# Optimization experiments

Hardware: AMD Instinct MI355X
Metric: run time of the kernel (lower is better)

The kernel has to match this reference:

```python
import jax, jax.numpy as jnp
import numpy as np

B, C, H, W = 16, 512, 64, 64   # C == e_dim
N_E = 256                       # codebook size
BETA = 0.25


def setup_inputs() -> dict:
    key = jax.random.key(0)
    k1, k2, k3 = jax.random.split(key, 3)
    z = jax.random.normal(k1, (B, C, H, W), dtype=jnp.float32)
    # nn.Embedding init: uniform(-1/n_e, 1/n_e)
    emb_weight = jax.random.uniform(k2, (N_E, C), dtype=jnp.float32,
                                    minval=-1.0 / N_E, maxval=1.0 / N_E)
    std_param = jnp.array(1.0, dtype=jnp.float32)
    means = jnp.zeros((3,), dtype=jnp.float32)
    conv_w = jax.random.normal(k3, (C, C), dtype=jnp.float32) * 0.02  # 1x1 conv kernel [out,in]
    conv_b = jnp.zeros((C,), dtype=jnp.float32)
    return {"z": z, "emb_weight": emb_weight, "std_param": std_param,
            "means": means, "conv_w": conv_w, "conv_b": conv_b}


def reference(z, emb_weight, std_param, means, conv_w, conv_b):
    # torch uses .item() on std/mean -> detached scalars
    std = jax.lax.stop_gradient(jnp.abs(std_param))
    mean = jax.lax.stop_gradient(jnp.mean(means))
    w = emb_weight * std + mean                      # [n_e, C] scaled codebook

    zf = z.transpose(0, 2, 3, 1).reshape(-1, C)       # [N, C], N = B*H*W
    # pairwise squared L2: ||z||^2 + ||w||^2 - 2 z.w
    d = (jnp.sum(zf * zf, axis=1, keepdims=True)
         + jnp.sum(w * w, axis=1)
         - 2.0 * zf @ w.T)                            # [N, n_e]
    idx = jnp.argmin(d, axis=1)                       # [N]
    one_hot = jax.nn.one_hot(idx, N_E, dtype=z.dtype) # [N, n_e]

    z_q = (one_hot @ w).reshape(B, H, W, C).transpose(0, 3, 1, 2)  # [B,C,H,W]

    sg = jax.lax.stop_gradient
    loss = jnp.mean((sg(z_q) - z) ** 2) + BETA * jnp.mean((z_q - sg(z)) ** 2)

    z_q = z + sg(z_q - z)                             # straight-through

    e_mean = jnp.mean(one_hot, axis=0)                # [n_e]
    perplexity = jnp.exp(-jnp.sum(e_mean * jnp.log(e_mean + 1e-10)))

    # 1x1 conv == channel matmul
    out = jnp.einsum('bchw,oc->bohw', z_q, conv_w) + conv_b[None, :, None, None]
    return out, loss, perplexity
```

## Files before the change

kernel.cpp:

```cpp
#include <hip/hip_runtime.h>


#define C_DIM 512
#define N_E   256
#define HW    4096
#define SAr   72

typedef unsigned short u16;
typedef u16   u16x4 __attribute__((ext_vector_type(4)));
typedef u16   u16x8 __attribute__((ext_vector_type(8)));
typedef short s16x8 __attribute__((ext_vector_type(8)));
typedef float f32x4 __attribute__((ext_vector_type(4)));

__device__ __forceinline__ u16 f2bf(float f) {
    unsigned u = __float_as_uint(f);
    return (u16)((u + 0x7FFFu + ((u >> 16) & 1u)) >> 16);
}

__global__ __launch_bounds__(256)
void prep(const float* __restrict__ emb, const float* __restrict__ stdp,
          const float* __restrict__ means, const float* __restrict__ convw,
          const float* __restrict__ convb,
          u16* __restrict__ wfrag, float* __restrict__ wnorm,
          float* __restrict__ M2T, float* __restrict__ accum,
          unsigned int* __restrict__ hist) {
    int t = threadIdx.x;
    float stdv  = fabsf(stdp[0]);
    float meanv = (means[0] + means[1] + means[2]) * (1.0f / 3.0f);

    if (blockIdx.x < 256) {
        int c = blockIdx.x;
        if (c == 0) {
            hist[t] = 0u;
            if (t < 2) accum[t] = 0.f;
        }
        float ss = 0.f;
        for (int k = t; k < C_DIM; k += 256) {
            float w = emb[c * C_DIM + k] * stdv + meanv;
            ss += w * w;
            int ntg  = c >> 4;
            int lane = (c & 15) | (((k >> 3) & 3) << 4);
            int ksg  = k >> 5;
            int j    = k & 7;
            wfrag[((ntg * 16 + ksg) * 64 + lane) * 8 + j] = f2bf(w);
        }
        #pragma unroll
        for (int m = 1; m < 64; m <<= 1) ss += __shfl_xor(ss, m, 64);
        __shared__ float red[4];
        if ((t & 63) == 0) red[t >> 6] = ss;
        __syncthreads();
        if (t == 0) wnorm[c] = red[0] + red[1] + red[2] + red[3];
    } else {
        __shared__ float cw[4][C_DIM];
        int o0 = (blockIdx.x - 256) * 4;
        for (int i = t; i < 4 * C_DIM; i += 256)
            cw[i >> 9][i & 511] = convw[(o0 + (i >> 9)) * C_DIM + (i & 511)];
        __syncthreads();
        float a0 = 0.f, a1 = 0.f, a2 = 0.f, a3 = 0.f;
        const float* er = emb + t * C_DIM;
        #pragma unroll 4
        for (int k = 0; k < C_DIM; k += 4) {
            f32x4 ev = *(const f32x4*)(er + k);
            #pragma unroll
            for (int jj = 0; jj < 4; ++jj) {
                float w = ev[jj] * stdv + meanv;
                a0 += cw[0][k + jj] * w;
                a1 += cw[1][k + jj] * w;
                a2 += cw[2][k + jj] * w;
                a3 += cw[3][k + jj] * w;
            }
        }
        M2T[(o0 + 0) * N_E + t] = a0 + convb[o0 + 0];
        M2T[(o0 + 1) * N_E + t] = a1 + convb[o0 + 1];
        M2T[(o0 + 2) * N_E + t] = a2 + convb[o0 + 2];
        M2T[(o0 + 3) * N_E + t] = a3 + convb[o0 + 3];
    }
}

__global__ __launch_bounds__(256, 4)
void argmin_out(const float* __restrict__ z, const u16* __restrict__ wfrag,
                const float* __restrict__ wnorm, const float* __restrict__ M2T,
                float* __restrict__ out,
                float* __restrict__ accum, unsigned int* __restrict__ hist) {
    __shared__ u16 Ab[2][64 * SAr];
    __shared__ unsigned long long lmin[64];
    __shared__ unsigned int lhist[N_E];
    __shared__ float lred[8];
    __shared__ u16 lcode[64];

    int tid = threadIdx.x;
    int wave = tid >> 6, lane = tid & 63;
    int nq = wave;
    int bb = blockIdx.x;
    const float* zb = z + (size_t)(bb >> 6) * (C_DIM * HW) + (bb & 63) * 64;

    if (tid < 64) lmin[tid] = ~0ull;
    lhist[tid] = 0u;

    f32x4 acc[4][4];
    #pragma unroll
    for (int mt = 0; mt < 4; ++mt)
        #pragma unroll
        for (int nt = 0; nt < 4; ++nt)
            acc[mt][nt] = (f32x4){0.f, 0.f, 0.f, 0.f};

    int t4 = tid & 15, cg = tid >> 4;
    const float* gsrc = zb + (size_t)(cg * 4) * HW + t4 * 4;
    int skey = (t4 >> 1) & 7;
    int wch  = (((cg >> 1) ^ skey) * 8) + ((cg & 1) * 4);
    float zs = 0.f;

    int m15 = lane & 15, quad = lane >> 4;
    const u16x8* wf8 = (const u16x8*)wfrag;

    f32x4 sv[4];
    #pragma unroll
    for (int i = 0; i < 4; ++i) sv[i] = *(const f32x4*)(gsrc + (size_t)i * HW);
    #pragma unroll
    for (int p = 0; p < 4; ++p) {
        u16x4 pk;
        #pragma unroll
        for (int i = 0; i < 4; ++i) { float f = sv[i][p]; zs += f * f; pk[i] = f2bf(f); }
        *(u16x4*)(&Ab[0][(t4 * 4 + p) * SAr + wch]) = pk;
    }

    for (int kc = 0; kc < 8; ++kc) {
        int cur = kc & 1;
        if (kc < 7) {
            const float* g2 = gsrc + (size_t)((kc + 1) * 64) * HW;
            #pragma unroll
            for (int i = 0; i < 4; ++i) sv[i] = *(const f32x4*)(g2 + (size_t)i * HW);
        }
        __syncthreads();
        #pragma unroll
        for (int ks = 0; ks < 2; ++ks) {
            s16x8 am[4];
            #pragma unroll
            for (int mt = 0; mt < 4; ++mt) {
                int rkey = (mt * 2 + (m15 >> 3)) & 7;
                int rch = (ks * 32 + quad * 8) ^ (rkey * 8);
                am[mt] = __builtin_bit_cast(s16x8,
                    *(const u16x8*)(&Ab[cur][(mt * 16 + m15) * SAr + rch]));
            }
            #pragma unroll
            for (int nt = 0; nt < 4; ++nt) {
                int ntg = nq * 4 + nt, ksg = kc * 2 + ks;
                s16x8 bfr = __builtin_bit_cast(s16x8, wf8[(ntg * 16 + ksg) * 64 + lane]);
                #pragma unroll
                for (int mt = 0; mt < 4; ++mt)
                    acc[mt][nt] = __builtin_amdgcn_mfma_f32_16x16x32_bf16(
                        am[mt], bfr, acc[mt][nt], 0, 0, 0);
            }
        }
        if (kc < 7) {
            #pragma unroll
            for (int p = 0; p < 4; ++p) {
                u16x4 pk;
                #pragma unroll
                for (int i = 0; i < 4; ++i) { float f = sv[i][p]; zs += f * f; pk[i] = f2bf(f); }
                *(u16x4*)(&Ab[cur ^ 1][(t4 * 4 + p) * SAr + wch]) = pk;
            }
        }
    }

    float wn[4];
    #pragma unroll
    for (int nt = 0; nt < 4; ++nt) wn[nt] = wnorm[(nq * 4 + nt) * 16 + m15];

    #pragma unroll
    for (int mt = 0; mt < 4; ++mt) {
        #pragma unroll
        for (int r = 0; r < 4; ++r) {
            unsigned long long key = ~0ull;
            #pragma unroll
            for (int nt = 0; nt < 4; ++nt) {
                float d = wn[nt] - 2.0f * acc[mt][nt][r];
                unsigned u = __float_as_uint(d);
                u ^= (u >> 31) ? 0xFFFFFFFFu : 0x80000000u;
                unsigned code = (unsigned)((nq * 4 + nt) * 16 + m15);
                unsigned long long k2 = ((unsigned long long)u << 32) | code;
                key = (k2 < key) ? k2 : key;
            }
            #pragma unroll
            for (int sm = 1; sm < 16; sm <<= 1) {
                unsigned long long o2 = (unsigned long long)__shfl_xor((long long)key, sm, 64);
                key = (o2 < key) ? o2 : key;
            }
            if (m15 == 0) {
                int pos = mt * 16 + quad * 4 + r;
                atomicMin(&lmin[pos], key);
            }
        }
    }
    __syncthreads();

    float dsum = 0.f;
    if (tid < 64) {
        unsigned long long key = lmin[tid];
        unsigned code = (unsigned)(key & 0xFFFFu);
        unsigned u = (unsigned)(key >> 32);
        u ^= (u >> 31) ? 0x80000000u : 0xFFFFFFFFu;
        dsum = __uint_as_float(u);
        lcode[tid] = (u16)code;
        atomicAdd(&lhist[code], 1u);
    }
    #pragma unroll
    for (int sm = 1; sm < 64; sm <<= 1) {
        dsum += __shfl_xor(dsum, sm, 64);
        zs   += __shfl_xor(zs, sm, 64);
    }
    if (lane == 0) { lred[wave] = dsum; lred[4 + wave] = zs; }
    __syncthreads();
    if (tid == 0) {
        atomicAdd(&accum[0], lred[4] + lred[5] + lred[6] + lred[7]);
        atomicAdd(&accum[1], lred[0]);
    }
    unsigned cnt = lhist[tid];
    if (cnt) atomicAdd(&hist[tid], cnt);

    int t4o = tid & 15, oo = tid >> 4;
    int ec[4];
    #pragma unroll
    for (int jj = 0; jj < 4; ++jj) ec[jj] = (int)lcode[t4o * 4 + jj];
    float* obase = out + ((size_t)(bb >> 6) * C_DIM + oo) * HW + (bb & 63) * 64 + t4o * 4;
    const float* m2 = M2T + oo * N_E;
    #pragma unroll 4
    for (int og = 0; og < C_DIM; og += 16) {
        f32x4 r;
        #pragma unroll
        for (int jj = 0; jj < 4; ++jj) r[jj] = m2[og * N_E + ec[jj]];
        *(f32x4*)(obase + (size_t)og * HW) = r;
    }
}

__global__ __launch_bounds__(256)
void fin_k(const float* __restrict__ accum, const unsigned int* __restrict__ hist,
           float* __restrict__ out) {
    int tid = threadIdx.x;
    float e = (float)hist[tid] * (1.0f / 65536.0f);
    float term = e * logf(e + 1e-10f);
    #pragma unroll
    for (int m = 1; m < 64; m <<= 1) term += __shfl_xor(term, m, 64);
    __shared__ float red[4];
    if ((tid & 63) == 0) red[tid >> 6] = term;
    __syncthreads();
    if (tid == 0) {
        float s = red[0] + red[1] + red[2] + red[3];
        out[33554432] = 1.25f * (accum[0] + accum[1]) * (1.0f / 33554432.0f);
        out[33554433] = expf(-s);
    }
}

extern "C" void kernel_launch(void* const* d_in, const int* in_sizes, int n_in,
                              void* d_out, int out_size, void* d_ws, size_t ws_size,
                              hipStream_t stream) {
    (void)in_sizes; (void)n_in; (void)out_size; (void)ws_size;
    const float* z     = (const float*)d_in[0];
    const float* emb   = (const float*)d_in[1];
    const float* stdp  = (const float*)d_in[2];
    const float* means = (const float*)d_in[3];
    const float* convw = (const float*)d_in[4];
    const float* convb = (const float*)d_in[5];

    char* ws = (char*)d_ws;
    u16*   wfrag = (u16*)(ws + 0);
    float* wnorm = (float*)(ws + 262144);
    float* M2T   = (float*)(ws + 263168);
    float* accum = (float*)(ws + 787456);
    unsigned int* hist = (unsigned int*)(ws + 787464);
    float* out = (float*)d_out;

    prep      <<<384,  256, 0, stream>>>(emb, stdp, means, convw, convb,
                                         wfrag, wnorm, M2T, accum, hist);
    argmin_out<<<1024, 256, 0, stream>>>(z, wfrag, wnorm, M2T, out, accum, hist);
    fin_k     <<<1,    256, 0, stream>>>(accum, hist, out);
}
```

Measured before the change: 325.7 us.

## Split argmin and output gather into separate kernels with single-wave argmin blocks

The fused kernel is split in two. A single-wave argmin kernel handles 32 pixels and computes distances to all 256 codes itself, so the per-block LDS atomicMin merge across waves goes away; it writes the chosen indices to a workspace buffer. A new output kernel caches one M2T column in LDS and writes each output channel row contiguously by gathering through the indices, and it also absorbs the old finalize kernel. This targets the strided, scattered output writes and the global-memory gathers from M2T, at the cost of an extra index round-trip, one more kernel boundary, and heavier per-wave register use (32 accumulator vectors).

After: 411.4 us. 26.3% more time.

```diff
diff --git a/kernel.cpp b/kernel.cpp
--- a/kernel.cpp
+++ b/kernel.cpp
@@ -4,7 +4,7 @@
 #define C_DIM 512
 #define N_E   256
 #define HW    4096
-#define SAr   72
+#define SAr2  40
 
 typedef unsigned short u16;
 typedef u16   u16x4 __attribute__((ext_vector_type(4)));
@@ -77,108 +77,82 @@
     }
 }
 
-__global__ __launch_bounds__(256, 4)
-void argmin_out(const float* __restrict__ z, const u16* __restrict__ wfrag,
-                const float* __restrict__ wnorm, const float* __restrict__ M2T,
-                float* __restrict__ out,
-                float* __restrict__ accum, unsigned int* __restrict__ hist) {
-    __shared__ u16 Ab[2][64 * SAr];
-    __shared__ unsigned long long lmin[64];
+__global__ __launch_bounds__(64, 2)
+void argmin32(const float* __restrict__ z, const u16* __restrict__ wfrag,
+              const float* __restrict__ wnorm, u16* __restrict__ idxs,
+              float* __restrict__ accum, unsigned int* __restrict__ hist) {
+    __shared__ u16 As[2][32 * SAr2];
+    __shared__ u16 lcode[32];
     __shared__ unsigned int lhist[N_E];
-    __shared__ float lred[8];
-    __shared__ u16 lcode[64];
-
-    int tid = threadIdx.x;
-    int wave = tid >> 6, lane = tid & 63;
-    int nq = wave;
+
+    int t = threadIdx.x;
+    int pg = t & 7, cg = t >> 3;
+    int m15 = t & 15, quad = t >> 4;
     int bb = blockIdx.x;
-    const float* zb = z + (size_t)(bb >> 6) * (C_DIM * HW) + (bb & 63) * 64;
-
-    if (tid < 64) lmin[tid] = ~0ull;
-    lhist[tid] = 0u;
-
-    f32x4 acc[4][4];
-    #pragma unroll
-    for (int mt = 0; mt < 4; ++mt)
-        #pragma unroll
-        for (int nt = 0; nt < 4; ++nt)
+    const float* zb = z + (size_t)(bb >> 7) * (C_DIM * HW) + (bb & 127) * 32;
+
+    for (int i = t; i < N_E; i += 64) lhist[i] = 0u;
+
+    f32x4 acc[2][16];
+    #pragma unroll
+    for (int mt = 0; mt < 2; ++mt)
+        #pragma unroll
+        for (int nt = 0; nt < 16; ++nt)
             acc[mt][nt] = (f32x4){0.f, 0.f, 0.f, 0.f};
 
-    int t4 = tid & 15, cg = tid >> 4;
-    const float* gsrc = zb + (size_t)(cg * 4) * HW + t4 * 4;
-    int skey = (t4 >> 1) & 7;
-    int wch  = (((cg >> 1) ^ skey) * 8) + ((cg & 1) * 4);
+    const u16x8* wf8 = (const u16x8*)wfrag;
     float zs = 0.f;
 
-    int m15 = lane & 15, quad = lane >> 4;
-    const u16x8* wf8 = (const u16x8*)wfrag;
-
-    f32x4 sv[4];
-    #pragma unroll
-    for (int i = 0; i < 4; ++i) sv[i] = *(const f32x4*)(gsrc + (size_t)i * HW);
-    #pragma unroll
-    for (int p = 0; p < 4; ++p) {
-        u16x4 pk;
-        #pragma unroll
-        for (int i = 0; i < 4; ++i) { float f = sv[i][p]; zs += f * f; pk[i] = f2bf(f); }
-        *(u16x4*)(&Ab[0][(t4 * 4 + p) * SAr + wch]) = pk;
-    }
-
-    for (int kc = 0; kc < 8; ++kc) {
-        int cur = kc & 1;
-        if (kc < 7) {
-            const float* g2 = gsrc + (size_t)((kc + 1) * 64) * HW;
-            #pragma unroll
-            for (int i = 0; i < 4; ++i) sv[i] = *(const f32x4*)(g2 + (size_t)i * HW);
-        }
-        __syncthreads();
-        #pragma unroll
-        for (int ks = 0; ks < 2; ++ks) {
-            s16x8 am[4];
-            #pragma unroll
-            for (int mt = 0; mt < 4; ++mt) {
-                int rkey = (mt * 2 + (m15 >> 3)) & 7;
-                int rch = (ks * 32 + quad * 8) ^ (rkey * 8);
-                am[mt] = __builtin_bit_cast(s16x8,
-                    *(const u16x8*)(&Ab[cur][(mt * 16 + m15) * SAr + rch]));
-            }
-            #pragma unroll
-            for (int nt = 0; nt < 4; ++nt) {
-                int ntg = nq * 4 + nt, ksg = kc * 2 + ks;
-                s16x8 bfr = __builtin_bit_cast(s16x8, wf8[(ntg * 16 + ksg) * 64 + lane]);
-                #pragma unroll
-                for (int mt = 0; mt < 4; ++mt)
-                    acc[mt][nt] = __builtin_amdgcn_mfma_f32_16x16x32_bf16(
-                        am[mt], bfr, acc[mt][nt], 0, 0, 0);
-            }
-        }
-        if (kc < 7) {
-            #pragma unroll
-            for (int p = 0; p < 4; ++p) {
-                u16x4 pk;
-                #pragma unroll
-                for (int i = 0; i < 4; ++i) { float f = sv[i][p]; zs += f * f; pk[i] = f2bf(f); }
-                *(u16x4*)(&Ab[cur ^ 1][(t4 * 4 + p) * SAr + wch]) = pk;
-            }
-        }
-    }
-
-    float wn[4];
-    #pragma unroll
-    for (int nt = 0; nt < 4; ++nt) wn[nt] = wnorm[(nq * 4 + nt) * 16 + m15];
-
-    #pragma unroll
-    for (int mt = 0; mt < 4; ++mt) {
+    f32x4 sv[2][4];
+    #pragma unroll
+    for (int i = 0; i < 4; ++i)
+        sv[0][i] = *(const f32x4*)(zb + (size_t)(cg * 4 + i) * HW + pg * 4);
+
+    #pragma unroll
+    for (int ksg = 0; ksg < 16; ++ksg) {
+        int cb = ksg & 1;
+        #pragma unroll
+        for (int p = 0; p < 4; ++p) {
+            u16x4 pk;
+            #pragma unroll
+            for (int i = 0; i < 4; ++i) { float f = sv[cb][i][p]; zs += f * f; pk[i] = f2bf(f); }
+            *(u16x4*)(&As[cb][(pg * 4 + p) * SAr2 + cg * 4]) = pk;
+        }
+        if (ksg < 15) {
+            #pragma unroll
+            for (int i = 0; i < 4; ++i)
+                sv[cb ^ 1][i] = *(const f32x4*)(zb + (size_t)((ksg + 1) * 32 + cg * 4 + i) * HW + pg * 4);
+        }
+        s16x8 am[2];
+        #pragma unroll
+        for (int mt = 0; mt < 2; ++mt)
+            am[mt] = __builtin_bit_cast(s16x8,
+                *(const u16x8*)(&As[cb][(mt * 16 + m15) * SAr2 + quad * 8]));
+        #pragma unroll
+        for (int nt = 0; nt < 16; ++nt) {
+            s16x8 bfr = __builtin_bit_cast(s16x8, wf8[(nt * 16 + ksg) * 64 + t]);
+            acc[0][nt] = __builtin_amdgcn_mfma_f32_16x16x32_bf16(am[0], bfr, acc[0][nt], 0, 0, 0);
+            acc[1][nt] = __builtin_amdgcn_mfma_f32_16x16x32_bf16(am[1], bfr, acc[1][nt], 0, 0, 0);
+        }
+    }
+
+    float wn[16];
+    #pragma unroll
+    for (int nt = 0; nt < 16; ++nt) wn[nt] = wnorm[nt * 16 + m15];
+
+    float dsum = 0.f;
+    #pragma unroll
+    for (int mt = 0; mt < 2; ++mt) {
         #pragma unroll
         for (int r = 0; r < 4; ++r) {
             unsigned long long key = ~0ull;
             #pragma unroll
-            for (int nt = 0; nt < 4; ++nt) {
+            for (int nt = 0; nt < 16; ++nt) {
                 float d = wn[nt] - 2.0f * acc[mt][nt][r];
                 unsigned u = __float_as_uint(d);
                 u ^= (u >> 31) ? 0xFFFFFFFFu : 0x80000000u;
-                unsigned code = (unsigned)((nq * 4 + nt) * 16 + m15);
-                unsigned long long k2 = ((unsigned long long)u << 32) | code;
+                unsigned long long k2 = ((unsigned long long)u << 32)
+                                      | (unsigned)(nt * 16 + m15);
                 key = (k2 < key) ? k2 : key;
             }
             #pragma unroll
@@ -188,66 +162,64 @@
             }
             if (m15 == 0) {
                 int pos = mt * 16 + quad * 4 + r;
-                atomicMin(&lmin[pos], key);
-            }
-        }
-    }
+                unsigned code = (unsigned)(key & 0xFFFFu);
+                unsigned u = (unsigned)(key >> 32);
+                u ^= (u >> 31) ? 0x80000000u : 0xFFFFFFFFu;
+                dsum += __uint_as_float(u);
+                lcode[pos] = (u16)code;
+                atomicAdd(&lhist[code], 1u);
+            }
+        }
+    }
+    #pragma unroll
+    for (int sm = 1; sm < 64; sm <<= 1) {
+        zs   += __shfl_xor(zs, sm, 64);
+        dsum += __shfl_xor(dsum, sm, 64);
+    }
+    if (t == 0) {
+        atomicAdd(&accum[0], zs);
+        atomicAdd(&accum[1], dsum);
+    }
+    if (t < 32) idxs[(bb >> 7) * HW + (bb & 127) * 32 + t] = lcode[t];
+    for (int i = t; i < N_E; i += 64) {
+        unsigned cnt = lhist[i];
+        if (cnt) atomicAdd(&hist[i], cnt);
+    }
+}
+
+__global__ __launch_bounds__(256)
+void out_k(const float* __restrict__ M2T, const u16* __restrict__ idxs,
+           float* __restrict__ out, const float* __restrict__ accum,
+           const unsigned int* __restrict__ hist) {
+    __shared__ float col[N_E];
+    int tid = threadIdx.x;
+    int bk = blockIdx.x;
+    int o = bk & 511, b = bk >> 9;
+    col[tid] = M2T[o * N_E + tid];
     __syncthreads();
-
-    float dsum = 0.f;
-    if (tid < 64) {
-        unsigned long long key = lmin[tid];
-        unsigned code = (unsigned)(key & 0xFFFFu);
-        unsigned u = (unsigned)(key >> 32);
-        u ^= (u >> 31) ? 0x80000000u : 0xFFFFFFFFu;
-        dsum = __uint_as_float(u);
-        lcode[tid] = (u16)code;
-        atomicAdd(&lhist[code], 1u);
-    }
-    #pragma unroll
-    for (int sm = 1; sm < 64; sm <<= 1) {
-        dsum += __shfl_xor(dsum, sm, 64);
-        zs   += __shfl_xor(zs, sm, 64);
-    }
-    if (lane == 0) { lred[wave] = dsum; lred[4 + wave] = zs; }
-    __syncthreads();
-    if (tid == 0) {
-        atomicAdd(&accum[0], lred[4] + lred[5] + lred[6] + lred[7]);
-        atomicAdd(&accum[1], lred[0]);
-    }
-    unsigned cnt = lhist[tid];
-    if (cnt) atomicAdd(&hist[tid], cnt);
-
-    int t4o = tid & 15, oo = tid >> 4;
-    int ec[4];
-    #pragma unroll
-    for (int jj = 0; jj < 4; ++jj) ec[jj] = (int)lcode[t4o * 4 + jj];
-    float* obase = out + ((size_t)(bb >> 6) * C_DIM + oo) * HW + (bb & 63) * 64 + t4o * 4;
-    const float* m2 = M2T + oo * N_E;
-    #pragma unroll 4
-    for (int og = 0; og < C_DIM; og += 16) {
+    size_t obase = (size_t)b * (C_DIM * HW) + (size_t)o * HW;
+    #pragma unroll
+    for (int j = 0; j < 4; ++j) {
+        int p4 = (j * 256 + tid) * 4;
+        u16x4 ids = *(const u16x4*)(idxs + b * HW + p4);
         f32x4 r;
         #pragma unroll
-        for (int jj = 0; jj < 4; ++jj) r[jj] = m2[og * N_E + ec[jj]];
-        *(f32x4*)(obase + (size_t)og * HW) = r;
-    }
-}
-
-__global__ __launch_bounds__(256)
-void fin_k(const float* __restrict__ accum, const unsigned int* __restrict__ hist,
-           float* __restrict__ out) {
-    int tid = threadIdx.x;
-    float e = (float)hist[tid] * (1.0f / 65536.0f);
-    float term = e * logf(e + 1e-10f);
-    #pragma unroll
-    for (int m = 1; m < 64; m <<= 1) term += __shfl_xor(term, m, 64);
-    __shared__ float red[4];
-    if ((tid & 63) == 0) red[tid >> 6] = term;
-    __syncthreads();
-    if (tid == 0) {
-        float s = red[0] + red[1] + red[2] + red[3];
-        out[33554432] = 1.25f * (accum[0] + accum[1]) * (1.0f / 33554432.0f);
-        out[33554433] = expf(-s);
+        for (int jj = 0; jj < 4; ++jj) r[jj] = col[ids[jj]];
+        *(f32x4*)(out + obase + p4) = r;
+    }
+    if (bk == 0) {
+        float e = (float)hist[tid] * (1.0f / 65536.0f);
+        float term = e * logf(e + 1e-10f);
+        #pragma unroll
+        for (int m = 1; m < 64; m <<= 1) term += __shfl_xor(term, m, 64);
+        __shared__ float red[4];
+        if ((tid & 63) == 0) red[tid >> 6] = term;
+        __syncthreads();
+        if (tid == 0) {
+            float s = red[0] + red[1] + red[2] + red[3];
+            out[33554432] = 1.25f * (accum[0] + accum[1]) * (1.0f / 33554432.0f);
+            out[33554433] = expf(-s);
+        }
     }
 }
 
@@ -266,12 +238,13 @@
     u16*   wfrag = (u16*)(ws + 0);
     float* wnorm = (float*)(ws + 262144);
     float* M2T   = (float*)(ws + 263168);
-    float* accum = (float*)(ws + 787456);
-    unsigned int* hist = (unsigned int*)(ws + 787464);
+    u16*   idxs  = (u16*)(ws + 787456);
+    float* accum = (float*)(ws + 918528);
+    unsigned int* hist = (unsigned int*)(ws + 918536);
     float* out = (float*)d_out;
 
-    prep      <<<384,  256, 0, stream>>>(emb, stdp, means, convw, convb,
-                                         wfrag, wnorm, M2T, accum, hist);
-    argmin_out<<<1024, 256, 0, stream>>>(z, wfrag, wnorm, M2T, out, accum, hist);
-    fin_k     <<<1,    256, 0, stream>>>(accum, hist, out);
-}
+    prep    <<<384,  256, 0, stream>>>(emb, stdp, means, convw, convb,
+                                       wfrag, wnorm, M2T, accum, hist);
+    argmin32<<<2048,  64, 0, stream>>>(z, wfrag, wnorm, idxs, accum, hist);
+    out_k   <<<8192, 256, 0, stream>>>(M2T, idxs, out, accum, hist);
+}
```
